# Kernel optimization log

Measured on AMD Instinct MI355X. Metric: run time of the kernel, lower is better.

The kernel has to match this reference:

```python
import jax, jax.numpy as jnp
import numpy as np

N, E, G = 50000, 400000, 64
DIN, HID, H, ED = 128, 32, 8, 5
HC = H * HID            # 256, conv3 out_channels (concat=False, heads=1)
LH, DOUT = 256, 32
NEG_SLOPE = 0.2


def setup_inputs() -> dict:
    key = jax.random.key(0)
    ks = jax.random.split(key, 32)
    rn = lambda k, s, sc=0.05: (jax.random.normal(k, s, jnp.float32) * sc)
    inp = {
        "x": jax.random.normal(ks[0], (N, DIN), jnp.float32),
        "edge_index": jax.random.randint(ks[1], (2, E), 0, N, jnp.int32),
        "edge_attr": jax.random.uniform(ks[2], (E, ED), jnp.float32),
        "batch": jnp.sort(jax.random.randint(ks[3], (N,), 0, G, jnp.int32)),
        # conv1: in=DIN, heads=H, out=HID, concat=True
        "W1": rn(ks[4], (DIN, H * HID)), "as1": rn(ks[5], (H, HID)), "ad1": rn(ks[6], (H, HID)),
        "We1": rn(ks[7], (ED, H * HID)), "ae1": rn(ks[8], (H, HID)), "b1": jnp.zeros((H * HID,), jnp.float32),
        # conv2: in=H*HID, heads=H, out=HID, concat=True
        "W2": rn(ks[9], (H * HID, H * HID)), "as2": rn(ks[10], (H, HID)), "ad2": rn(ks[11], (H, HID)),
        "We2": rn(ks[12], (ED, H * HID)), "ae2": rn(ks[13], (H, HID)), "b2": jnp.zeros((H * HID,), jnp.float32),
        # conv3: in=H*HID, heads=1, out=HC, concat=False
        "W3": rn(ks[14], (H * HID, HC)), "as3": rn(ks[15], (1, HC)), "ad3": rn(ks[16], (1, HC)),
        "We3": rn(ks[17], (ED, HC)), "ae3": rn(ks[18], (1, HC)), "b3": jnp.zeros((HC,), jnp.float32),
        # MLP head
        "fcW1": rn(ks[19], (HC, LH)), "fcb1": jnp.zeros((LH,), jnp.float32),
        "fcW2": rn(ks[20], (LH, DOUT)), "fcb2": jnp.zeros((DOUT,), jnp.float32),
    }
    return inp


def gat_layer(x, src, dst, ea, W, att_s, att_d, We, att_e, bias, heads, out_ch, concat):
    n = x.shape[0]
    h = (x @ W).reshape(n, heads, out_ch)                 # [N,H,C]
    e = (ea @ We).reshape(-1, heads, out_ch)              # [E,H,C]
    a_s = (h * att_s).sum(-1)                             # [N,H]
    a_d = (h * att_d).sum(-1)                             # [N,H]
    a_e = (e * att_e).sum(-1)                             # [E,H]
    alpha = jax.nn.leaky_relu(a_s[src] + a_d[dst] + a_e, NEG_SLOPE)  # [E,H]
    m = jax.ops.segment_max(alpha, dst, num_segments=n)   # segment softmax over dst
    p = jnp.exp(alpha - m[dst])
    denom = jax.ops.segment_sum(p, dst, num_segments=n)
    w = p / (denom[dst] + 1e-16)                          # [E,H]
    msg = h[src] * w[:, :, None]                          # [E,H,C]
    out = jax.ops.segment_sum(msg, dst, num_segments=n)   # [N,H,C]
    out = out.reshape(n, heads * out_ch) if concat else out.mean(axis=1)
    return out + bias


def reference(x, edge_index, edge_attr, batch,
              W1, as1, ad1, We1, ae1, b1,
              W2, as2, ad2, We2, ae2, b2,
              W3, as3, ad3, We3, ae3, b3,
              fcW1, fcb1, fcW2, fcb2):
    src, dst = edge_index[0], edge_index[1]
    h = jax.nn.elu(gat_layer(x, src, dst, edge_attr, W1, as1, ad1, We1, ae1, b1, H, HID, True))
    h = jax.nn.elu(gat_layer(h, src, dst, edge_attr, W2, as2, ad2, We2, ae2, b2, H, HID, True))
    h = jax.nn.elu(gat_layer(h, src, dst, edge_attr, W3, as3, ad3, We3, ae3, b3, 1, HC, False))
    h = jax.nn.gelu(h @ fcW1 + fcb1, approximate=False) @ fcW2 + fcb2   # [N,DOUT]
    # global_mean_pool over batch ids
    sums = jax.ops.segment_sum(h, batch, num_segments=G)
    cnt = jax.ops.segment_sum(jnp.ones((h.shape[0],), h.dtype), batch, num_segments=G)
    return sums / jnp.maximum(cnt, 1.0)[:, None]
```

## Files before the change

kernel.cpp:

```cpp
#include <hip/hip_runtime.h>
#include <math.h>


#define N_NODES 50000
#define N_EDGES 400000
#define N_GRAPH 64
#define DIN     128
#define NHC     256
#define DOUT    32

typedef _Float16 f16x8 __attribute__((ext_vector_type(8)));
typedef _Float16 f16x4 __attribute__((ext_vector_type(4)));
typedef float    f32x4 __attribute__((ext_vector_type(4)));

#define LDP2 72

__device__ __forceinline__ void fma_mix_lo(float& acc, float pj, int w) {
    asm volatile("v_fma_mix_f32 %0, %1, %2, %0 op_sel:[0,0,0] op_sel_hi:[0,1,0]"
                 : "+v"(acc) : "v"(pj), "v"(w));
}
__device__ __forceinline__ void fma_mix_hi(float& acc, float pj, int w) {
    asm volatile("v_fma_mix_f32 %0, %1, %2, %0 op_sel:[0,1,0] op_sel_hi:[0,1,0]"
                 : "+v"(acc) : "v"(pj), "v"(w));
}

__global__ __launch_bounds__(256) void mfma_gemm_kernel(
    const _Float16* __restrict__ Ah, const _Float16* __restrict__ Bh,
    const float* __restrict__ bias, _Float16* __restrict__ Ch,
    const float* __restrict__ asl, const float* __restrict__ adl,
    float* __restrict__ asb, float* __restrict__ adb,
    const int* __restrict__ batch, float* __restrict__ pooled,
    int nrow, int K, int mode)
{
    __shared__ __align__(16) _Float16 sAh[128][LDP2];
    __shared__ __align__(16) _Float16 sBh[64][LDP2];

    const int tid = threadIdx.x, lane = tid & 63, wid = tid >> 6;
    const int wm = wid & 1, wn = wid >> 1;

    int xt, yt;
    if (gridDim.x == 4) {
        int bid = blockIdx.x + (blockIdx.y << 2);
        yt = (bid >> 5) * 8 + (bid & 7);
        xt = (bid >> 3) & 3;
    } else { xt = blockIdx.x; yt = blockIdx.y; }
    const int row0 = yt * 128, col0 = xt * 64;
    if (row0 >= nrow) return;

    const int frow = lane & 15, fk = (lane >> 4) * 8;

    f32x4 acc[4][2] = {};
    f16x8 pA[4], pB[2];

#pragma unroll
    for (int p = 0; p < 4; p++) {
        int idx = tid + p * 256;
        int r = idx >> 3, ch = (idx & 7) * 8;
        int gr = row0 + r;
        pA[p] = (gr < nrow) ? *(const f16x8*)(Ah + (long)gr * K + ch) : (f16x8)0;
    }
#pragma unroll
    for (int p = 0; p < 2; p++) {
        int idx = tid + p * 256;
        int r = idx >> 3, ch = (idx & 7) * 8;
        pB[p] = *(const f16x8*)(Bh + (long)(col0 + r) * K + ch);
    }

    for (int k0 = 0; k0 < K; k0 += 64) {
#pragma unroll
        for (int p = 0; p < 4; p++) {
            int idx = tid + p * 256;
            *(f16x8*)&sAh[idx >> 3][(idx & 7) * 8] = pA[p];
        }
#pragma unroll
        for (int p = 0; p < 2; p++) {
            int idx = tid + p * 256;
            *(f16x8*)&sBh[idx >> 3][(idx & 7) * 8] = pB[p];
        }
        __syncthreads();

        if (k0 + 64 < K) {
            int kn = k0 + 64;
#pragma unroll
            for (int p = 0; p < 4; p++) {
                int idx = tid + p * 256;
                int r = idx >> 3, ch = (idx & 7) * 8;
                int gr = row0 + r;
                pA[p] = (gr < nrow) ? *(const f16x8*)(Ah + (long)gr * K + kn + ch) : (f16x8)0;
            }
#pragma unroll
            for (int p = 0; p < 2; p++) {
                int idx = tid + p * 256;
                int r = idx >> 3, ch = (idx & 7) * 8;
                pB[p] = *(const f16x8*)(Bh + (long)(col0 + r) * K + kn + ch);
            }
        }

#pragma unroll
        for (int sub = 0; sub < 2; sub++) {
            const int fks = fk + sub * 32;
            f16x8 bh[2];
#pragma unroll
            for (int nt = 0; nt < 2; nt++)
                bh[nt] = *(const f16x8*)&sBh[wn * 32 + nt * 16 + frow][fks];
#pragma unroll
            for (int mt = 0; mt < 4; mt++) {
                f16x8 ah = *(const f16x8*)&sAh[wm * 64 + mt * 16 + frow][fks];
#pragma unroll
                for (int nt = 0; nt < 2; nt++)
                    acc[mt][nt] = __builtin_amdgcn_mfma_f32_16x16x32_f16(ah, bh[nt], acc[mt][nt], 0, 0, 0);
            }
        }
        __syncthreads();
    }

    const int crow0 = row0 + wm * 64 + (lane >> 4) * 4;
    const int ccol0 = col0 + wn * 32 + (lane & 15);

    if (mode == 0) {
#pragma unroll
        for (int mt = 0; mt < 4; mt++)
#pragma unroll
            for (int nt = 0; nt < 2; nt++) {
                int col = ccol0 + nt * 16;
#pragma unroll
                for (int r = 0; r < 4; r++) {
                    int row = crow0 + mt * 16 + r;
                    if (row < nrow) Ch[(long)row * 256 + col] = (_Float16)acc[mt][nt][r];
                }
            }
        if (asl != nullptr) {
            const float asl0 = asl[ccol0], asl1 = asl[ccol0 + 16];
            const float adl0 = adl[ccol0], adl1 = adl[ccol0 + 16];
            const int headw = (col0 + wn * 32) >> 5;
#pragma unroll
            for (int mt = 0; mt < 4; mt++) {
#pragma unroll
                for (int r = 0; r < 4; r++) {
                    float s = acc[mt][0][r] * asl0 + acc[mt][1][r] * asl1;
                    float d = acc[mt][0][r] * adl0 + acc[mt][1][r] * adl1;
                    s += __shfl_xor(s, 1); s += __shfl_xor(s, 2);
                    s += __shfl_xor(s, 4); s += __shfl_xor(s, 8);
                    d += __shfl_xor(d, 1); d += __shfl_xor(d, 2);
                    d += __shfl_xor(d, 4); d += __shfl_xor(d, 8);
                    if ((lane & 15) == 0) {
                        int row = crow0 + mt * 16 + r;
                        if (row < nrow) {
                            asb[row * 8 + headw] = s;
                            adb[row * 8 + headw] = d;
                        }
                    }
                }
            }
        }
    } else {
        float* pool = (float*)&sAh[0][0];
        const int g0 = batch[row0];
        const int rlast = (row0 + 127 < nrow) ? row0 + 127 : nrow - 1;
        const int gspan = batch[rlast] - g0 + 1;
        const bool fits = (gspan <= 16);
        for (int i = tid; i < 16 * 64; i += 256) pool[i] = 0.f;
        __syncthreads();

        const float b0 = bias[ccol0], b1 = bias[ccol0 + 16];
        const int lc0 = ccol0 - col0, lc1 = lc0 + 16;
        float sum0 = 0.f, sum1 = 0.f;
        int curg = -1;
#pragma unroll
        for (int mt = 0; mt < 4; mt++) {
#pragma unroll
            for (int r = 0; r < 4; r++) {
                int row = crow0 + mt * 16 + r;
                if (row >= nrow) continue;
                int g = batch[row];
                if (g != curg) {
                    if (curg >= 0) {
                        if (fits) {
                            atomicAdd(&pool[(curg - g0) * 64 + lc0], sum0);
                            atomicAdd(&pool[(curg - g0) * 64 + lc1], sum1);
                        } else {
                            atomicAdd(&pooled[curg * 256 + ccol0], sum0);
                            atomicAdd(&pooled[curg * 256 + ccol0 + 16], sum1);
                        }
                    }
                    curg = g; sum0 = 0.f; sum1 = 0.f;
                }
                float v0 = acc[mt][0][r] + b0;
                float v1 = acc[mt][1][r] + b1;
                sum0 += 0.5f * v0 * (1.f + erff(v0 * 0.7071067811865475f));
                sum1 += 0.5f * v1 * (1.f + erff(v1 * 0.7071067811865475f));
            }
        }
        if (curg >= 0) {
            if (fits) {
                atomicAdd(&pool[(curg - g0) * 64 + lc0], sum0);
                atomicAdd(&pool[(curg - g0) * 64 + lc1], sum1);
            } else {
                atomicAdd(&pooled[curg * 256 + ccol0], sum0);
                atomicAdd(&pooled[curg * 256 + ccol0 + 16], sum1);
            }
        }
        __syncthreads();
        if (fits) {
            for (int i = tid; i < gspan * 64; i += 256) {
                float val = pool[i];
                if (val != 0.f)
                    atomicAdd(&pooled[(g0 + (i >> 6)) * 256 + col0 + (i & 63)], val);
            }
        }
    }
}

__global__ __launch_bounds__(256) void sum8_kernel(
    float* __restrict__ asb3, float* __restrict__ adb3, int n)
{
    int r = blockIdx.x * 256 + threadIdx.x;
    if (r >= n) return;
    const float4* a = (const float4*)(asb3 + (long)r * 8);
    float4 a0 = a[0], a1 = a[1];
    asb3[(long)r * 8] = a0.x + a0.y + a0.z + a0.w + a1.x + a1.y + a1.z + a1.w;
    const float4* b = (const float4*)(adb3 + (long)r * 8);
    float4 b0 = b[0], b1 = b[1];
    adb3[(long)r * 8] = b0.x + b0.y + b0.z + b0.w + b1.x + b1.y + b1.z + b1.w;
}

#define J0 1600000
#define J1 32768
#define J2 65536
#define J3 65536
#define J4 65536
#define J5 16384
#define J6 N_NODES
#define J7 64
#define J9 85
#define JTOT (J0+J1+J2+J3+J4+J5+J6+J7+J9)

__device__ __forceinline__ void t_one(const float* W, _Float16* Bh,
                                      int id, int K, int realN)
{
    int n = id / K, k = id - n * K;
    Bh[id] = (_Float16)W[(long)k * realN + n];
}

__global__ __launch_bounds__(256) void prep_kernel(
    const float* __restrict__ x,
    const float* __restrict__ W1, const float* __restrict__ W2, const float* __restrict__ W3,
    const float* __restrict__ F1,
    const float* __restrict__ We1, const float* __restrict__ ae1,
    const float* __restrict__ We2, const float* __restrict__ ae2,
    const float* __restrict__ We3, const float* __restrict__ ae3,
    _Float16* __restrict__ xh,
    _Float16* __restrict__ W1th, _Float16* __restrict__ W2th,
    _Float16* __restrict__ W3th, _Float16* __restrict__ F1th,
    float* __restrict__ pooled, int* __restrict__ deg, int* __restrict__ gcnt,
    float* __restrict__ MeAll)
{
    int idx = blockIdx.x * 256 + threadIdx.x;
    if (idx < J0) {
        float4 v = ((const float4*)x)[idx];
        f16x4 h;
        h[0] = (_Float16)v.x; h[1] = (_Float16)v.y;
        h[2] = (_Float16)v.z; h[3] = (_Float16)v.w;
        *(f16x4*)(xh + (long)idx * 4) = h;
        return;
    }
    idx -= J0;
    if (idx < J1) { t_one(W1, W1th, idx, DIN, NHC); return; }
    idx -= J1;
    if (idx < J2) { t_one(W2, W2th, idx, NHC, NHC); return; }
    idx -= J2;
    if (idx < J3) { t_one(W3, W3th, idx, NHC, NHC); return; }
    idx -= J3;
    if (idx < J4) { t_one(F1, F1th, idx, NHC, NHC); return; }
    idx -= J4;
    if (idx < J5) { pooled[idx] = 0.f; return; }
    idx -= J5;
    if (idx < J6) { deg[idx] = 0; return; }
    idx -= J6;
    if (idx < J7) { gcnt[idx] = 0; return; }
    idx -= J7;
    if (idx < J9) {
        int l, j, hh, H, C;
        if (idx < 40)      { l = 0; H = 8; C = 32;  j = idx >> 3; hh = idx & 7; }
        else if (idx < 80) { l = 1; H = 8; C = 32;  int r = idx - 40; j = r >> 3; hh = r & 7; }
        else               { l = 2; H = 1; C = 256; j = idx - 80; hh = 0; }
        const float* We = (l == 0) ? We1 : (l == 1) ? We2 : We3;
        const float* ae = (l == 0) ? ae1 : (l == 1) ? ae2 : ae3;
        float s = 0.f;
        for (int c = 0; c < C; c++) s += We[j * NHC + hh * C + c] * ae[hh * C + c];
        MeAll[l * 40 + j * H + hh] = s;
        return;
    }
}

__global__ __launch_bounds__(256) void count_hist_kernel(
    const int* __restrict__ ei, const int* __restrict__ batch,
    int* __restrict__ deg, int* __restrict__ gcnt, int E, int N)
{
    __shared__ int hist[N_GRAPH];
    int t = threadIdx.x;
    if (t < N_GRAPH) hist[t] = 0;
    __syncthreads();
    int i = blockIdx.x * 256 + t;
    if (i < E) atomicAdd(&deg[ei[E + i]], 1);
    if (i < N) atomicAdd(&hist[batch[i]], 1);
    __syncthreads();
    if (t < N_GRAPH && hist[t] > 0) atomicAdd(&gcnt[t], hist[t]);
}

__global__ __launch_bounds__(256) void scan_block_kernel(
    const int* __restrict__ deg, int* __restrict__ rowstart, int* __restrict__ partial, int n)
{
    __shared__ int s[256];
    int i = blockIdx.x * 256 + threadIdx.x;
    int v = (i < n) ? deg[i] : 0;
    s[threadIdx.x] = v;
    __syncthreads();
    for (int off = 1; off < 256; off <<= 1) {
        int t = (threadIdx.x >= off) ? s[threadIdx.x - off] : 0;
        __syncthreads();
        s[threadIdx.x] += t;
        __syncthreads();
    }
    if (i < n) rowstart[i] = s[threadIdx.x] - v;
    if (threadIdx.x == 255) partial[blockIdx.x] = s[255];
}

__global__ __launch_bounds__(256) void scan_add2_kernel(
    int* __restrict__ rowstart, const int* __restrict__ partial, int* __restrict__ cursor,
    int n, int E, int nb)
{
    __shared__ int sp[256];
    int t = threadIdx.x;
    sp[t] = (t < nb) ? partial[t] : 0;
    __syncthreads();
    for (int off = 1; off < 256; off <<= 1) {
        int v = (t >= off) ? sp[t - off] : 0;
        __syncthreads();
        sp[t] += v;
        __syncthreads();
    }
    int add = (blockIdx.x == 0) ? 0 : sp[blockIdx.x - 1];
    int i = blockIdx.x * 256 + t;
    if (i < n) {
        int v = rowstart[i] + add;
        rowstart[i] = v;
        cursor[i] = v;
    }
    if (i == 0) rowstart[n] = E;
}

__global__ __launch_bounds__(256) void fill_kernel(
    const int* __restrict__ ei, int* __restrict__ cursor, int2* __restrict__ csr2, int E)
{
    int e = blockIdx.x * 256 + threadIdx.x;
    if (e >= E) return;
    int dst = ei[E + e];
    int pos = atomicAdd(&cursor[dst], 1);
    csr2[pos] = make_int2(ei[e], e);
}

__global__ __launch_bounds__(256) void aec_kernel(
    const int2* __restrict__ csr2, const float* __restrict__ ea,
    const float* __restrict__ MeAll,
    int* __restrict__ csr, _Float16* __restrict__ aec, int E)
{
    int pos = blockIdx.x * 256 + threadIdx.x;
    if (pos >= E) return;
    int2 se = csr2[pos];
    csr[pos] = se.x;
    const float* eap = ea + (long)se.y * 5;
    float e0 = eap[0], e1 = eap[1], e2 = eap[2], e3 = eap[3], e4 = eap[4];
#pragma unroll
    for (int l = 0; l < 2; l++) {
        const float* Me = MeAll + l * 40;
        f16x8 v;
#pragma unroll
        for (int hh = 0; hh < 8; hh++) {
            float s = e0 * Me[hh] + e1 * Me[8 + hh] + e2 * Me[16 + hh]
                    + e3 * Me[24 + hh] + e4 * Me[32 + hh];
            v[hh] = (_Float16)s;
        }
        *(f16x8*)(aec + (long)l * N_EDGES * 8 + (long)pos * 8) = v;
    }
    const float* Me2 = MeAll + 80;
    float s2 = e0 * Me2[0] + e1 * Me2[1] + e2 * Me2[2] + e3 * Me2[3] + e4 * Me2[4];
    f16x8 v2;
#pragma unroll
    for (int hh = 0; hh < 8; hh++) v2[hh] = (_Float16)s2;
    *(f16x8*)(aec + (long)2 * N_EDGES * 8 + (long)pos * 8) = v2;
}

__global__ __launch_bounds__(256) void gat_agg_kernel(
    const int* __restrict__ rowstart, const int* __restrict__ csr,
    const _Float16* __restrict__ aec, const float* __restrict__ asb,
    const float* __restrict__ adb,
    const _Float16* __restrict__ h, const float* __restrict__ bias,
    _Float16* __restrict__ Oh, int H, int clog2)
{
    int node = blockIdx.x * 4 + (threadIdx.x >> 6);
    if (node >= N_NODES) return;
    const int lane = threadIdx.x & 63;
    const int half = lane >> 5;
    const int c8   = (lane & 31) * 8;
    const int hc   = c8 >> clog2;
    const int heff = lane & (H - 1);
    const int grp  = lane >> 3;

    const float adn = adb[node * 8 + heff];
    const int beg = rowstart[node], end = rowstart[node + 1];

    float acc[8] = {};
    float den = 0.f;

    for (int i = beg; i < end; i += 8) {
        int idx = i + grp;
        const bool valid = (idx < end);
        if (!valid) idx = end - 1;
        const int sj = csr[idx];
        const float ae = (float)aec[(long)idx * 8 + heff];
        float al = asb[sj * 8 + heff] + adn + ae;
        al = fmaxf(al, 0.2f * al);
        const float pv = valid ? __expf(al) : 0.f;
#pragma unroll
        for (int jj = 0; jj < 4; jj++) {
            const int j = jj * 2 + half;
            const float pj = __shfl(pv, j * 8 + hc);
            const int srcj = __shfl(sj, j * 8);
            const int4 hw = *(const int4*)(h + (long)srcj * NHC + c8);
            den += pj;
            fma_mix_lo(acc[0], pj, hw.x); fma_mix_hi(acc[1], pj, hw.x);
            fma_mix_lo(acc[2], pj, hw.y); fma_mix_hi(acc[3], pj, hw.y);
            fma_mix_lo(acc[4], pj, hw.z); fma_mix_hi(acc[5], pj, hw.z);
            fma_mix_lo(acc[6], pj, hw.w); fma_mix_hi(acc[7], pj, hw.w);
        }
    }

    den += __shfl_xor(den, 32);
#pragma unroll
    for (int k = 0; k < 8; k++)
        acc[k] += __shfl_xor(acc[k], 32);

    if (half == 0) {
        const float w = 1.0f / (den + 1e-16f);
        const float4 b0 = *(const float4*)(bias + c8);
        const float4 b1 = *(const float4*)(bias + c8 + 4);
        const float bb[8] = {b0.x, b0.y, b0.z, b0.w, b1.x, b1.y, b1.z, b1.w};
        f16x8 oh;
#pragma unroll
        for (int k = 0; k < 8; k++) {
            float v = acc[k] * w + bb[k];
            v = (v > 0.f) ? v : (__expf(v) - 1.f);
            oh[k] = (_Float16)v;
        }
        *(f16x8*)(Oh + (long)node * NHC + c8) = oh;
    }
}

__global__ void final_kernel(const float* __restrict__ pooled, const int* __restrict__ gcnt,
                             const float* __restrict__ fcW2, const float* __restrict__ fcb2,
                             float* __restrict__ out)
{
    int g = blockIdx.x;
    int j = threadIdx.x;
    if (j >= DOUT) return;
    float s = 0.f;
    for (int k = 0; k < NHC; k++) s += pooled[g * NHC + k] * fcW2[k * DOUT + j];
    int c = gcnt[g];
    out[g * DOUT + j] = (c > 0) ? (s / (float)c + fcb2[j]) : 0.f;
}

extern "C" void kernel_launch(void* const* d_in, const int* in_sizes, int n_in,
                              void* d_out, int out_size, void* d_ws, size_t ws_size,
                              hipStream_t stream)
{
    const float* x    = (const float*)d_in[0];
    const int*   ei   = (const int*)  d_in[1];
    const float* ea   = (const float*)d_in[2];
    const int*   bat  = (const int*)  d_in[3];
    const float* W[3]   = {(const float*)d_in[4],  (const float*)d_in[10], (const float*)d_in[16]};
    const float* Asl[3] = {(const float*)d_in[5],  (const float*)d_in[11], (const float*)d_in[17]};
    const float* Adl[3] = {(const float*)d_in[6],  (const float*)d_in[12], (const float*)d_in[18]};
    const float* Wel[3] = {(const float*)d_in[7],  (const float*)d_in[13], (const float*)d_in[19]};
    const float* Ael[3] = {(const float*)d_in[8],  (const float*)d_in[14], (const float*)d_in[20]};
    const float* Bil[3] = {(const float*)d_in[9],  (const float*)d_in[15], (const float*)d_in[21]};
    const float* fcW1 = (const float*)d_in[22];
    const float* fcb1 = (const float*)d_in[23];
    const float* fcW2 = (const float*)d_in[24];
    const float* fcb2 = (const float*)d_in[25];

    char* w = (char*)d_ws;
    _Float16* h    = (_Float16*)w;     w += (size_t)N_NODES * NHC * 2;
    _Float16* xh   = (_Float16*)w;     w += (size_t)N_NODES * DIN * 2;
    _Float16* xbh  = (_Float16*)w;     w += (size_t)N_NODES * NHC * 2;
    float*    asb  = (float*)w;        w += (size_t)N_NODES * 8 * 4;
    float*    adb  = (float*)w;        w += (size_t)N_NODES * 8 * 4;
    float*    asb3 = (float*)w;        w += (size_t)N_NODES * 8 * 4;
    float*    adb3 = (float*)w;        w += (size_t)N_NODES * 8 * 4;
    float*    MeAll= (float*)w;        w += 120 * 4;
    float*    pooled=(float*)w;        w += (size_t)N_GRAPH * NHC * 4;
    _Float16* W1th = (_Float16*)w;     w += (size_t)NHC * DIN * 2;
    _Float16* W2th = (_Float16*)w;     w += (size_t)NHC * NHC * 2;
    _Float16* W3th = (_Float16*)w;     w += (size_t)NHC * NHC * 2;
    _Float16* F1th = (_Float16*)w;     w += (size_t)NHC * NHC * 2;
    int* gcnt     = (int*)w;           w += N_GRAPH * 4;
    int* deg      = (int*)w;           w += (size_t)N_NODES * 4;
    int* rowstart = (int*)w;           w += (size_t)(N_NODES + 1) * 4;
    int* cursor   = (int*)w;           w += (size_t)N_NODES * 4;
    int* partial  = (int*)w;           w += 256 * 4;
    w = (char*)(((size_t)w + 15) & ~(size_t)15);
    int2* csr2    = (int2*)w;          w += (size_t)N_EDGES * 8;
    int* csr      = (int*)w;           w += (size_t)N_EDGES * 4;
    w = (char*)(((size_t)w + 15) & ~(size_t)15);
    _Float16* aec = (_Float16*)w;      w += (size_t)3 * N_EDGES * 8 * 2;

    const int NB = (N_NODES + 255) / 256;

    prep_kernel<<<(JTOT + 255) / 256, 256, 0, stream>>>(
        x, W[0], W[1], W[2], fcW1,
        Wel[0], Ael[0], Wel[1], Ael[1], Wel[2], Ael[2],
        xh, W1th, W2th, W3th, F1th,
        pooled, deg, gcnt, MeAll);
    count_hist_kernel<<<(N_EDGES + 255) / 256, 256, 0, stream>>>(ei, bat, deg, gcnt, N_EDGES, N_NODES);
    scan_block_kernel<<<NB, 256, 0, stream>>>(deg, rowstart, partial, N_NODES);
    scan_add2_kernel<<<NB, 256, 0, stream>>>(rowstart, partial, cursor, N_NODES, N_EDGES, NB);
    fill_kernel<<<(N_EDGES + 255) / 256, 256, 0, stream>>>(ei, cursor, csr2, N_EDGES);
    aec_kernel<<<(N_EDGES + 255) / 256, 256, 0, stream>>>(csr2, ea, MeAll, csr, aec, N_EDGES);

    const int Hs[3] = {8, 8, 1};
    const int CL[3] = {5, 5, 8};
    const int Ks[3] = {DIN, NHC, NHC};

    const dim3 ggrid(4, 392);

    const _Float16* curh = xh;
    const _Float16* Wth[3] = {W1th, W2th, W3th};
    for (int l = 0; l < 3; l++) {
        const int H = Hs[l];
        const bool h1 = (l == 2);
        mfma_gemm_kernel<<<ggrid, 256, 0, stream>>>(
            curh, Wth[l], nullptr, h,
            Asl[l], Adl[l], h1 ? asb3 : asb, h1 ? adb3 : adb,
            nullptr, nullptr,
            N_NODES, Ks[l], 0);
        if (h1)
            sum8_kernel<<<NB, 256, 0, stream>>>(asb3, adb3, N_NODES);
        gat_agg_kernel<<<(N_NODES + 3) / 4, 256, 0, stream>>>(
            rowstart, csr, aec + (size_t)l * N_EDGES * 8,
            h1 ? asb3 : asb, h1 ? adb3 : adb, h, Bil[l], xbh, H, CL[l]);
        curh = xbh;
    }

    mfma_gemm_kernel<<<ggrid, 256, 0, stream>>>(
        xbh, F1th, fcb1, nullptr,
        nullptr, nullptr, nullptr, nullptr,
        bat, pooled,
        N_NODES, NHC, 3);
    final_kernel<<<N_GRAPH, 64, 0, stream>>>(pooled, gcnt, fcW2, fcb2, (float*)d_out);
}
```

Measured before the change: 428.8 us.

## Fuse graph-build preprocessing kernels into one cooperative persistent kernel

Merges the prep, degree-count/histogram, two-stage scan, CSR fill, and edge-attention precompute kernels into a single cooperative kernel launched with 1024 blocks, separating phases with grid-wide syncs. The goal is to remove five kernel launch gaps and their tail effects in the preprocessing stage. In exchange, each phase now uses grid-stride loops over fewer blocks, and grid.sync barriers add their own cost. The scan phases still need NBC=196 blocks, which fits within the 1024-block grid.

```diff
diff --git a/kernel.cpp b/kernel.cpp
--- a/kernel.cpp
+++ b/kernel.cpp
@@ -1,5 +1,8 @@
 #include <hip/hip_runtime.h>
+#include <hip/hip_cooperative_groups.h>
 #include <math.h>
+
+namespace cg = cooperative_groups;
 
 
 #define N_NODES 50000
@@ -234,161 +237,157 @@
 #define J7 64
 #define J9 85
 #define JTOT (J0+J1+J2+J3+J4+J5+J6+J7+J9)
+#define NBC  ((N_NODES + 255) / 256)
+
+struct BuildArgs {
+    const float* x;
+    const float* W1; const float* W2; const float* W3; const float* F1;
+    const float* We1; const float* ae1;
+    const float* We2; const float* ae2;
+    const float* We3; const float* ae3;
+    const int* ei; const int* batch; const float* ea;
+    _Float16* xh;
+    _Float16* W1th; _Float16* W2th; _Float16* W3th; _Float16* F1th;
+    float* pooled; int* deg; int* gcnt; float* MeAll;
+    int* rowstart; int* cursor; int* partial;
+    int2* csr2; int* csr; _Float16* aec;
+};
 
 __device__ __forceinline__ void t_one(const float* W, _Float16* Bh,
-                                      int id, int K, int realN)
-{
-    int n = id / K, k = id - n * K;
-    Bh[id] = (_Float16)W[(long)k * realN + n];
-}
-
-__global__ __launch_bounds__(256) void prep_kernel(
-    const float* __restrict__ x,
-    const float* __restrict__ W1, const float* __restrict__ W2, const float* __restrict__ W3,
-    const float* __restrict__ F1,
-    const float* __restrict__ We1, const float* __restrict__ ae1,
-    const float* __restrict__ We2, const float* __restrict__ ae2,
-    const float* __restrict__ We3, const float* __restrict__ ae3,
-    _Float16* __restrict__ xh,
-    _Float16* __restrict__ W1th, _Float16* __restrict__ W2th,
-    _Float16* __restrict__ W3th, _Float16* __restrict__ F1th,
-    float* __restrict__ pooled, int* __restrict__ deg, int* __restrict__ gcnt,
-    float* __restrict__ MeAll)
-{
-    int idx = blockIdx.x * 256 + threadIdx.x;
+                                      long id, int K, int realN)
+{
+    long n = id / K, k = id - n * K;
+    Bh[id] = (_Float16)W[k * realN + n];
+}
+
+__device__ __forceinline__ void prep_job(const BuildArgs& a, long idx)
+{
     if (idx < J0) {
-        float4 v = ((const float4*)x)[idx];
+        float4 v = ((const float4*)a.x)[idx];
         f16x4 h;
         h[0] = (_Float16)v.x; h[1] = (_Float16)v.y;
         h[2] = (_Float16)v.z; h[3] = (_Float16)v.w;
-        *(f16x4*)(xh + (long)idx * 4) = h;
+        *(f16x4*)(a.xh + idx * 4) = h;
         return;
     }
     idx -= J0;
-    if (idx < J1) { t_one(W1, W1th, idx, DIN, NHC); return; }
+    if (idx < J1) { t_one(a.W1, a.W1th, idx, DIN, NHC); return; }
     idx -= J1;
-    if (idx < J2) { t_one(W2, W2th, idx, NHC, NHC); return; }
+    if (idx < J2) { t_one(a.W2, a.W2th, idx, NHC, NHC); return; }
     idx -= J2;
-    if (idx < J3) { t_one(W3, W3th, idx, NHC, NHC); return; }
+    if (idx < J3) { t_one(a.W3, a.W3th, idx, NHC, NHC); return; }
     idx -= J3;
-    if (idx < J4) { t_one(F1, F1th, idx, NHC, NHC); return; }
+    if (idx < J4) { t_one(a.F1, a.F1th, idx, NHC, NHC); return; }
     idx -= J4;
-    if (idx < J5) { pooled[idx] = 0.f; return; }
+    if (idx < J5) { a.pooled[idx] = 0.f; return; }
     idx -= J5;
-    if (idx < J6) { deg[idx] = 0; return; }
+    if (idx < J6) { a.deg[idx] = 0; return; }
     idx -= J6;
-    if (idx < J7) { gcnt[idx] = 0; return; }
+    if (idx < J7) { a.gcnt[idx] = 0; return; }
     idx -= J7;
     if (idx < J9) {
         int l, j, hh, H, C;
-        if (idx < 40)      { l = 0; H = 8; C = 32;  j = idx >> 3; hh = idx & 7; }
-        else if (idx < 80) { l = 1; H = 8; C = 32;  int r = idx - 40; j = r >> 3; hh = r & 7; }
-        else               { l = 2; H = 1; C = 256; j = idx - 80; hh = 0; }
-        const float* We = (l == 0) ? We1 : (l == 1) ? We2 : We3;
-        const float* ae = (l == 0) ? ae1 : (l == 1) ? ae2 : ae3;
+        int id = (int)idx;
+        if (id < 40)      { l = 0; H = 8; C = 32;  j = id >> 3; hh = id & 7; }
+        else if (id < 80) { l = 1; H = 8; C = 32;  int r = id - 40; j = r >> 3; hh = r & 7; }
+        else              { l = 2; H = 1; C = 256; j = id - 80; hh = 0; }
+        const float* We = (l == 0) ? a.We1 : (l == 1) ? a.We2 : a.We3;
+        const float* ae = (l == 0) ? a.ae1 : (l == 1) ? a.ae2 : a.ae3;
         float s = 0.f;
         for (int c = 0; c < C; c++) s += We[j * NHC + hh * C + c] * ae[hh * C + c];
-        MeAll[l * 40 + j * H + hh] = s;
+        a.MeAll[l * 40 + j * H + hh] = s;
         return;
     }
 }
 
-__global__ __launch_bounds__(256) void count_hist_kernel(
-    const int* __restrict__ ei, const int* __restrict__ batch,
-    int* __restrict__ deg, int* __restrict__ gcnt, int E, int N)
-{
-    __shared__ int hist[N_GRAPH];
-    int t = threadIdx.x;
-    if (t < N_GRAPH) hist[t] = 0;
+__global__ __launch_bounds__(256) void build_kernel(BuildArgs a)
+{
+    cg::grid_group grid = cg::this_grid();
+    const int tid = threadIdx.x;
+    const long stride = (long)gridDim.x * 256;
+    __shared__ int sh[256];
+
+    for (long idx = (long)blockIdx.x * 256 + tid; idx < JTOT; idx += stride)
+        prep_job(a, idx);
+    grid.sync();
+
+    if (tid < N_GRAPH) sh[tid] = 0;
     __syncthreads();
-    int i = blockIdx.x * 256 + t;
-    if (i < E) atomicAdd(&deg[ei[E + i]], 1);
-    if (i < N) atomicAdd(&hist[batch[i]], 1);
+    for (long b = (long)blockIdx.x * 256 + tid; b < N_EDGES; b += stride)
+        atomicAdd(&a.deg[a.ei[N_EDGES + b]], 1);
+    for (long b = (long)blockIdx.x * 256 + tid; b < N_NODES; b += stride)
+        atomicAdd(&sh[a.batch[b]], 1);
     __syncthreads();
-    if (t < N_GRAPH && hist[t] > 0) atomicAdd(&gcnt[t], hist[t]);
-}
-
-__global__ __launch_bounds__(256) void scan_block_kernel(
-    const int* __restrict__ deg, int* __restrict__ rowstart, int* __restrict__ partial, int n)
-{
-    __shared__ int s[256];
-    int i = blockIdx.x * 256 + threadIdx.x;
-    int v = (i < n) ? deg[i] : 0;
-    s[threadIdx.x] = v;
-    __syncthreads();
-    for (int off = 1; off < 256; off <<= 1) {
-        int t = (threadIdx.x >= off) ? s[threadIdx.x - off] : 0;
+    if (tid < N_GRAPH && sh[tid] > 0) atomicAdd(&a.gcnt[tid], sh[tid]);
+    grid.sync();
+
+    if (blockIdx.x < NBC) {
+        int i = blockIdx.x * 256 + tid;
+        int v = (i < N_NODES) ? a.deg[i] : 0;
+        sh[tid] = v;
         __syncthreads();
-        s[threadIdx.x] += t;
+        for (int off = 1; off < 256; off <<= 1) {
+            int t = (tid >= off) ? sh[tid - off] : 0;
+            __syncthreads();
+            sh[tid] += t;
+            __syncthreads();
+        }
+        if (i < N_NODES) a.rowstart[i] = sh[tid] - v;
+        if (tid == 255) a.partial[blockIdx.x] = sh[255];
+    }
+    grid.sync();
+
+    if (blockIdx.x < NBC) {
+        sh[tid] = (tid < NBC) ? a.partial[tid] : 0;
         __syncthreads();
-    }
-    if (i < n) rowstart[i] = s[threadIdx.x] - v;
-    if (threadIdx.x == 255) partial[blockIdx.x] = s[255];
-}
-
-__global__ __launch_bounds__(256) void scan_add2_kernel(
-    int* __restrict__ rowstart, const int* __restrict__ partial, int* __restrict__ cursor,
-    int n, int E, int nb)
-{
-    __shared__ int sp[256];
-    int t = threadIdx.x;
-    sp[t] = (t < nb) ? partial[t] : 0;
-    __syncthreads();
-    for (int off = 1; off < 256; off <<= 1) {
-        int v = (t >= off) ? sp[t - off] : 0;
-        __syncthreads();
-        sp[t] += v;
-        __syncthreads();
-    }
-    int add = (blockIdx.x == 0) ? 0 : sp[blockIdx.x - 1];
-    int i = blockIdx.x * 256 + t;
-    if (i < n) {
-        int v = rowstart[i] + add;
-        rowstart[i] = v;
-        cursor[i] = v;
-    }
-    if (i == 0) rowstart[n] = E;
-}
-
-__global__ __launch_bounds__(256) void fill_kernel(
-    const int* __restrict__ ei, int* __restrict__ cursor, int2* __restrict__ csr2, int E)
-{
-    int e = blockIdx.x * 256 + threadIdx.x;
-    if (e >= E) return;
-    int dst = ei[E + e];
-    int pos = atomicAdd(&cursor[dst], 1);
-    csr2[pos] = make_int2(ei[e], e);
-}
-
-__global__ __launch_bounds__(256) void aec_kernel(
-    const int2* __restrict__ csr2, const float* __restrict__ ea,
-    const float* __restrict__ MeAll,
-    int* __restrict__ csr, _Float16* __restrict__ aec, int E)
-{
-    int pos = blockIdx.x * 256 + threadIdx.x;
-    if (pos >= E) return;
-    int2 se = csr2[pos];
-    csr[pos] = se.x;
-    const float* eap = ea + (long)se.y * 5;
-    float e0 = eap[0], e1 = eap[1], e2 = eap[2], e3 = eap[3], e4 = eap[4];
-#pragma unroll
-    for (int l = 0; l < 2; l++) {
-        const float* Me = MeAll + l * 40;
-        f16x8 v;
-#pragma unroll
-        for (int hh = 0; hh < 8; hh++) {
-            float s = e0 * Me[hh] + e1 * Me[8 + hh] + e2 * Me[16 + hh]
-                    + e3 * Me[24 + hh] + e4 * Me[32 + hh];
-            v[hh] = (_Float16)s;
-        }
-        *(f16x8*)(aec + (long)l * N_EDGES * 8 + (long)pos * 8) = v;
-    }
-    const float* Me2 = MeAll + 80;
-    float s2 = e0 * Me2[0] + e1 * Me2[1] + e2 * Me2[2] + e3 * Me2[3] + e4 * Me2[4];
-    f16x8 v2;
-#pragma unroll
-    for (int hh = 0; hh < 8; hh++) v2[hh] = (_Float16)s2;
-    *(f16x8*)(aec + (long)2 * N_EDGES * 8 + (long)pos * 8) = v2;
+        for (int off = 1; off < 256; off <<= 1) {
+            int t = (tid >= off) ? sh[tid - off] : 0;
+            __syncthreads();
+            sh[tid] += t;
+            __syncthreads();
+        }
+        int add = (blockIdx.x == 0) ? 0 : sh[blockIdx.x - 1];
+        int i = blockIdx.x * 256 + tid;
+        if (i < N_NODES) {
+            int v = a.rowstart[i] + add;
+            a.rowstart[i] = v;
+            a.cursor[i] = v;
+        }
+        if (i == 0) a.rowstart[N_NODES] = N_EDGES;
+    }
+    grid.sync();
+
+    for (long e = (long)blockIdx.x * 256 + tid; e < N_EDGES; e += stride) {
+        int dst = a.ei[N_EDGES + e];
+        int pos = atomicAdd(&a.cursor[dst], 1);
+        a.csr2[pos] = make_int2(a.ei[e], (int)e);
+    }
+    grid.sync();
+
+    for (long pos = (long)blockIdx.x * 256 + tid; pos < N_EDGES; pos += stride) {
+        int2 se = a.csr2[pos];
+        a.csr[pos] = se.x;
+        const float* eap = a.ea + (long)se.y * 5;
+        float e0 = eap[0], e1 = eap[1], e2 = eap[2], e3 = eap[3], e4 = eap[4];
+#pragma unroll
+        for (int l = 0; l < 2; l++) {
+            const float* Me = a.MeAll + l * 40;
+            f16x8 v;
+#pragma unroll
+            for (int hh = 0; hh < 8; hh++) {
+                float s = e0 * Me[hh] + e1 * Me[8 + hh] + e2 * Me[16 + hh]
+                        + e3 * Me[24 + hh] + e4 * Me[32 + hh];
+                v[hh] = (_Float16)s;
+            }
+            *(f16x8*)(a.aec + (long)l * N_EDGES * 8 + pos * 8) = v;
+        }
+        const float* Me2 = a.MeAll + 80;
+        float s2 = e0 * Me2[0] + e1 * Me2[1] + e2 * Me2[2] + e3 * Me2[3] + e4 * Me2[4];
+        f16x8 v2;
+#pragma unroll
+        for (int hh = 0; hh < 8; hh++) v2[hh] = (_Float16)s2;
+        *(f16x8*)(a.aec + (long)2 * N_EDGES * 8 + pos * 8) = v2;
+    }
 }
 
 __global__ __launch_bounds__(256) void gat_agg_kernel(
@@ -516,16 +515,22 @@
 
     const int NB = (N_NODES + 255) / 256;
 
-    prep_kernel<<<(JTOT + 255) / 256, 256, 0, stream>>>(
-        x, W[0], W[1], W[2], fcW1,
-        Wel[0], Ael[0], Wel[1], Ael[1], Wel[2], Ael[2],
-        xh, W1th, W2th, W3th, F1th,
-        pooled, deg, gcnt, MeAll);
-    count_hist_kernel<<<(N_EDGES + 255) / 256, 256, 0, stream>>>(ei, bat, deg, gcnt, N_EDGES, N_NODES);
-    scan_block_kernel<<<NB, 256, 0, stream>>>(deg, rowstart, partial, N_NODES);
-    scan_add2_kernel<<<NB, 256, 0, stream>>>(rowstart, partial, cursor, N_NODES, N_EDGES, NB);
-    fill_kernel<<<(N_EDGES + 255) / 256, 256, 0, stream>>>(ei, cursor, csr2, N_EDGES);
-    aec_kernel<<<(N_EDGES + 255) / 256, 256, 0, stream>>>(csr2, ea, MeAll, csr, aec, N_EDGES);
+    BuildArgs ba;
+    ba.x = x;
+    ba.W1 = W[0]; ba.W2 = W[1]; ba.W3 = W[2]; ba.F1 = fcW1;
+    ba.We1 = Wel[0]; ba.ae1 = Ael[0];
+    ba.We2 = Wel[1]; ba.ae2 = Ael[1];
+    ba.We3 = Wel[2]; ba.ae3 = Ael[2];
+    ba.ei = ei; ba.batch = bat; ba.ea = ea;
+    ba.xh = xh;
+    ba.W1th = W1th; ba.W2th = W2th; ba.W3th = W3th; ba.F1th = F1th;
+    ba.pooled = pooled; ba.deg = deg; ba.gcnt = gcnt; ba.MeAll = MeAll;
+    ba.rowstart = rowstart; ba.cursor = cursor; ba.partial = partial;
+    ba.csr2 = csr2; ba.csr = csr; ba.aec = aec;
+
+    void* kp[] = { (void*)&ba };
+    hipLaunchCooperativeKernel((const void*)build_kernel,
+                               dim3(1024), dim3(256), kp, 0, stream);
 
     const int Hs[3] = {8, 8, 1};
     const int CL[3] = {5, 5, 8};
```

After: 1.045 ms. +143.8%, slower.
